# Optimization experiments

Measured on AMD Instinct MI355X. Metric: run time of the kernel, lower is better.

## Reference

```python
import jax, jax.numpy as jnp
import numpy as np

N_EMBED = 288
HEAD_SIZE = 32


def setup_inputs() -> dict:
    key = jax.random.key(0)
    kx, kk, kq, kv = jax.random.split(key, 4)
    B, T, C = 16, 2048, N_EMBED
    scale = 1.0 / np.sqrt(C)
    return {
        "x": jax.random.normal(kx, (B, T, C), dtype=jnp.float32),
        # Linear(n_embed, head_size, bias=False) weights, stored as [C, head_size]
        "Wk": jax.random.normal(kk, (C, HEAD_SIZE), dtype=jnp.float32) * scale,
        "Wq": jax.random.normal(kq, (C, HEAD_SIZE), dtype=jnp.float32) * scale,
        "Wv": jax.random.normal(kv, (C, HEAD_SIZE), dtype=jnp.float32) * scale,
    }


def reference(x, Wk, Wq, Wv):
    # x: [B, T, C]
    k = x @ Wk  # [B, T, hs]
    q = x @ Wq
    v = x @ Wv
    # NOTE: source computes k @ q^T (not q @ k^T) -- reproduce faithfully.
    weights = jnp.einsum("bth,bsh->bts", k, q) * (HEAD_SIZE ** -0.5)  # [B, T, T]
    T = x.shape[1]
    causal = jnp.tril(jnp.ones((T, T), dtype=bool))
    weights = jnp.where(causal, weights, -jnp.inf)
    weights = jax.nn.softmax(weights, axis=-1)
    return weights @ v  # [B, T, hs]
```

## Files before the change

kernel.cpp:

```cpp
#include <hip/hip_runtime.h>

typedef __bf16 bf16;
typedef __attribute__((ext_vector_type(8))) __bf16 bf16x8;
typedef __attribute__((ext_vector_type(4))) float f32x4;

#define BATCH 16
#define SEQ   2048
#define CEMB  288
#define HS    32
#define NROWS (BATCH * SEQ)

#define XSTR 296

__global__ __launch_bounds__(384) void proj_kernel(
    const float* __restrict__ x, const float* __restrict__ Wk,
    const float* __restrict__ Wq, const float* __restrict__ Wv,
    bf16* __restrict__ Kx, bf16* __restrict__ Qm, bf16* __restrict__ VT)
{
    __shared__ __align__(16) bf16 Xl[32 * XSTR];

    const int tid  = threadIdx.x;
    const int wv   = tid >> 6;
    const int lane = tid & 63;
    const int quad = lane >> 4;
    const int ln   = lane & 15;
    const int dsel = wv >> 1;
    const int half = wv & 1;

    const float SCALE = 0.25519486439582695f;

    const float* Wsrc = (dsel == 0) ? Wk : ((dsel == 1) ? Wq : Wv);
    const float mul = (dsel == 0) ? SCALE : 1.0f;
    bf16x8 wfrag[9];
    for (int kc = 0; kc < 9; ++kc) {
        bf16x8 f;
#pragma unroll
        for (int j = 0; j < 8; ++j) {
            float w = Wsrc[(kc * 32 + quad * 8 + j) * HS + half * 16 + ln];
            f[j] = (bf16)(w * mul);
        }
        wfrag[kc] = f;
    }

    const int wgRowBase = blockIdx.x * 128;
    for (int it = 0; it < 4; ++it) {
        __syncthreads();
        const int rb = wgRowBase + it * 32;
#pragma unroll
        for (int i = 0; i < 6; ++i) {
            int f = tid + 384 * i;
            int row = f / 72;
            int c4  = f - row * 72;
            f32x4 v = ((const f32x4*)x)[(rb + row) * 72 + c4];
            bf16* d = &Xl[row * XSTR + c4 * 4];
            d[0] = (bf16)v[0]; d[1] = (bf16)v[1];
            d[2] = (bf16)v[2]; d[3] = (bf16)v[3];
        }
        __syncthreads();

#pragma unroll
        for (int m = 0; m < 2; ++m) {
            f32x4 acc = {0.f, 0.f, 0.f, 0.f};
#pragma unroll
            for (int kc = 0; kc < 9; ++kc) {
                bf16x8 a = *(const bf16x8*)&Xl[(m * 16 + ln) * XSTR + kc * 32 + quad * 8];
                acc = __builtin_amdgcn_mfma_f32_16x16x32_bf16(a, wfrag[kc], acc, 0, 0, 0);
            }
#pragma unroll
            for (int reg = 0; reg < 4; ++reg) {
                int gr = rb + m * 16 + quad * 4 + reg;
                bf16 val = (bf16)acc[reg];
                if (dsel == 0) {
                    Kx[gr * HS + half * 16 + ln] = val;
                } else if (dsel == 1) {
                    Qm[gr * HS + half * 16 + ln] = val;
                } else {
                    VT[(gr >> 11) * (HS * SEQ) + (half * 16 + ln) * SEQ + (gr & 2047)] = val;
                }
            }
        }
    }
}

#define QSTR 40
#define PSTR 56

__constant__ unsigned char MAP_TILE[40] = {
    4,5,6,7, 8,8,9,9, 10,10,11,11, 12,12,12, 13,13,13, 14,14,14, 15,15,15,
    3,7,11,15, 2,6,10,14, 1,5,9,13, 0,4,8,12 };
__constant__ unsigned char MAP_CHUNK[40] = {
    0,0,0,0, 0,1,0,1, 0,1,0,1, 0,1,2, 0,1,2, 0,1,2, 0,1,2,
    0,1,2,3, 0,1,2,3, 0,1,2,3, 0,1,2,3 };

__global__ __launch_bounds__(256) void attn_kernel(
    const bf16* __restrict__ Kx, const bf16* __restrict__ Qm,
    const bf16* __restrict__ VT,
    float* __restrict__ Opart, float* __restrict__ Lpart)
{
    __shared__ __align__(16) bf16 qT[32 * QSTR];
    __shared__ __align__(16) bf16 vT[32 * QSTR];
    __shared__ __align__(16) bf16 Pl[4][2][16 * PSTR];

    const int tid  = threadIdx.x;
    const int w    = tid >> 6;
    const int lane = tid & 63;
    const int quad = lane >> 4;
    const int ln   = lane & 15;

    const int bid   = blockIdx.x;
    const int b     = bid & 15;
    const int u     = bid >> 4;
    const int tile  = MAP_TILE[u];
    const int chunk = MAP_CHUNK[u];
    const int t0    = tile * 128;
    const int cs    = chunk * 512;
    const int ce    = min(cs + 512, t0 + 128);

    const bf16* Kb = Kx + b * SEQ * HS;
    const bf16* Qb = Qm + b * SEQ * HS;
    const bf16* Vb = VT + b * HS * SEQ;

    int tsub[2];
    bf16x8 kfrag[2];
#pragma unroll
    for (int m = 0; m < 2; ++m) {
        tsub[m] = t0 + w * 32 + m * 16;
        kfrag[m] = *(const bf16x8*)&Kb[(tsub[m] + ln) * HS + quad * 8];
    }
    bf16x8 ones;
#pragma unroll
    for (int j = 0; j < 8; ++j) ones[j] = (bf16)1.0f;

    f32x4 Of[2][2] = {};
    f32x4 Lf[2]    = {};

    for (int s0 = cs; s0 < ce; s0 += 32) {
        __syncthreads();
        if (tid < 128) {
            int sr = tid >> 2, h8 = (tid & 3) * 8;
            *(bf16x8*)&qT[sr * QSTR + h8] = *(const bf16x8*)&Qb[(s0 + sr) * HS + h8];
        } else {
            int t2 = tid - 128;
            int hr = t2 >> 2, s8 = (t2 & 3) * 8;
            *(bf16x8*)&vT[hr * QSTR + s8] = *(const bf16x8*)&Vb[hr * SEQ + s0 + s8];
        }
        __syncthreads();

#pragma unroll
        for (int m = 0; m < 2; ++m) {
            if (s0 >= tsub[m] + 16) continue;
            const bool diag = (s0 + 31 > tsub[m]);

            f32x4 S[2];
#pragma unroll
            for (int ss = 0; ss < 2; ++ss) {
                bf16x8 qf = *(const bf16x8*)&qT[(ss * 16 + ln) * QSTR + quad * 8];
                f32x4 z = {0.f, 0.f, 0.f, 0.f};
                S[ss] = __builtin_amdgcn_mfma_f32_16x16x32_bf16(kfrag[m], qf, z, 0, 0, 0);
            }

            bf16* P = &Pl[w][m][0];
#pragma unroll
            for (int ss = 0; ss < 2; ++ss) {
#pragma unroll
                for (int reg = 0; reg < 4; ++reg) {
                    float p = __builtin_amdgcn_exp2f(S[ss][reg]);
                    if (diag) {
                        int s = s0 + ss * 16 + ln;
                        int t = tsub[m] + quad * 4 + reg;
                        p = (s <= t) ? p : 0.0f;
                    }
                    P[(quad * 4 + reg) * PSTR + ss * 16 + ln] = (bf16)p;
                }
            }

            bf16x8 ap = *(const bf16x8*)&P[ln * PSTR + quad * 8];
            bf16x8 v0 = *(const bf16x8*)&vT[ln * QSTR + quad * 8];
            bf16x8 v1 = *(const bf16x8*)&vT[(16 + ln) * QSTR + quad * 8];
            Of[m][0] = __builtin_amdgcn_mfma_f32_16x16x32_bf16(ap, v0, Of[m][0], 0, 0, 0);
            Of[m][1] = __builtin_amdgcn_mfma_f32_16x16x32_bf16(ap, v1, Of[m][1], 0, 0, 0);
            Lf[m]    = __builtin_amdgcn_mfma_f32_16x16x32_bf16(ap, ones, Lf[m], 0, 0, 0);
        }
    }

#pragma unroll
    for (int m = 0; m < 2; ++m) {
        if (cs >= tsub[m] + 16) continue;
#pragma unroll
        for (int reg = 0; reg < 4; ++reg) {
            int gr = b * SEQ + tsub[m] + quad * 4 + reg;
            float* od = Opart + ((size_t)chunk * NROWS + gr) * HS;
            od[ln]      = Of[m][0][reg];
            od[16 + ln] = Of[m][1][reg];
            if (ln == 0) Lpart[chunk * NROWS + gr] = Lf[m][reg];
        }
    }
}

__global__ __launch_bounds__(256) void combine_kernel(
    const float* __restrict__ Opart, const float* __restrict__ Lpart,
    float* __restrict__ out)
{
    int idx = blockIdx.x * 256 + threadIdx.x;
    int gr = idx >> 3, h4 = idx & 7;
    int t  = gr & 2047;
    int nc = (t >> 9) + 1;
    f32x4 acc = {0.f, 0.f, 0.f, 0.f};
    float l = 0.f;
    for (int c = 0; c < nc; ++c) {
        acc += ((const f32x4*)Opart)[((size_t)c * NROWS + gr) * 8 + h4];
        l   += Lpart[c * NROWS + gr];
    }
    f32x4 r = acc / l;
    ((f32x4*)out)[idx] = r;
}

extern "C" void kernel_launch(void* const* d_in, const int* in_sizes, int n_in,
                              void* d_out, int out_size, void* d_ws, size_t ws_size,
                              hipStream_t stream) {
    (void)in_sizes; (void)n_in; (void)out_size; (void)ws_size;
    const float* x  = (const float*)d_in[0];
    const float* Wk = (const float*)d_in[1];
    const float* Wq = (const float*)d_in[2];
    const float* Wv = (const float*)d_in[3];

    char* ws = (char*)d_ws;
    bf16*  Kx    = (bf16*)(ws);
    bf16*  Qm    = (bf16*)(ws + 2097152);
    bf16*  VT    = (bf16*)(ws + 4194304);
    float* Opart = (float*)(ws + 6291456);
    float* Lpart = (float*)(ws + 23068672);
    float* out   = (float*)d_out;

    hipLaunchKernelGGL(proj_kernel, dim3(256), dim3(384), 0, stream,
                       x, Wk, Wq, Wv, Kx, Qm, VT);
    hipLaunchKernelGGL(attn_kernel, dim3(640), dim3(256), 0, stream,
                       Kx, Qm, VT, Opart, Lpart);
    hipLaunchKernelGGL(combine_kernel, dim3(1024), dim3(256), 0, stream,
                       Opart, Lpart, out);
}
```

Measured before the change: 111.8 us.

## Give each wave its own query tile and keep P in registers via 16x16x16 MFMA

The attention kernel now assigns each wave an independent 32-row tile and chunk, so workgroup-wide barriers and shared staging of Q/V are gone. K/Q/V fragments are loaded directly from global memory, with the next block prefetched into registers. When the 16x16x16 bf16 MFMA is available, the exp'd score fragment is fed straight back as the A operand, with no LDS round trip for P. Fully masked sub-blocks are skipped. The projection kernel also launches twice as many workgroups with half the rows each, to spread work more widely. The trade-offs are more global loads per wave (no sharing through LDS) and more register use.

After: 119.5 us. 1.07x slower.

```diff
diff --git a/kernel.cpp b/kernel.cpp
--- a/kernel.cpp
+++ b/kernel.cpp
@@ -2,6 +2,8 @@
 
 typedef __bf16 bf16;
 typedef __attribute__((ext_vector_type(8))) __bf16 bf16x8;
+typedef __attribute__((ext_vector_type(4))) __bf16 bf16x4;
+typedef __attribute__((ext_vector_type(4))) short s16x4;
 typedef __attribute__((ext_vector_type(4))) float f32x4;
 
 #define BATCH 16
@@ -9,6 +11,13 @@
 #define CEMB  288
 #define HS    32
 #define NROWS (BATCH * SEQ)
+
+#if __has_builtin(__builtin_amdgcn_mfma_f32_16x16x16bf16_1k)
+#define HAVE_MFMA16 1
+#define MFMA16(a, b, c) __builtin_amdgcn_mfma_f32_16x16x16bf16_1k((a), (b), (c), 0, 0, 0)
+#else
+#define HAVE_MFMA16 0
+#endif
 
 #define XSTR 296
 
@@ -42,8 +51,8 @@
         wfrag[kc] = f;
     }
 
-    const int wgRowBase = blockIdx.x * 128;
-    for (int it = 0; it < 4; ++it) {
+    const int wgRowBase = blockIdx.x * 64;
+    for (int it = 0; it < 2; ++it) {
         __syncthreads();
         const int rb = wgRowBase + it * 32;
 #pragma unroll
@@ -82,24 +91,16 @@
     }
 }
 
-#define QSTR 40
-#define PSTR 56
-
-__constant__ unsigned char MAP_TILE[40] = {
-    4,5,6,7, 8,8,9,9, 10,10,11,11, 12,12,12, 13,13,13, 14,14,14, 15,15,15,
-    3,7,11,15, 2,6,10,14, 1,5,9,13, 0,4,8,12 };
-__constant__ unsigned char MAP_CHUNK[40] = {
-    0,0,0,0, 0,1,0,1, 0,1,0,1, 0,1,2, 0,1,2, 0,1,2, 0,1,2,
-    0,1,2,3, 0,1,2,3, 0,1,2,3, 0,1,2,3 };
+#define PSTR 40
 
 __global__ __launch_bounds__(256) void attn_kernel(
     const bf16* __restrict__ Kx, const bf16* __restrict__ Qm,
     const bf16* __restrict__ VT,
     float* __restrict__ Opart, float* __restrict__ Lpart)
 {
-    __shared__ __align__(16) bf16 qT[32 * QSTR];
-    __shared__ __align__(16) bf16 vT[32 * QSTR];
-    __shared__ __align__(16) bf16 Pl[4][2][16 * PSTR];
+#if !HAVE_MFMA16
+    __shared__ __align__(16) bf16 Pl[4][16 * PSTR];
+#endif
 
     const int tid  = threadIdx.x;
     const int w    = tid >> 6;
@@ -107,92 +108,150 @@
     const int quad = lane >> 4;
     const int ln   = lane & 15;
 
-    const int bid   = blockIdx.x;
-    const int b     = bid & 15;
-    const int u     = bid >> 4;
-    const int tile  = MAP_TILE[u];
-    const int chunk = MAP_CHUNK[u];
-    const int t0    = tile * 128;
-    const int cs    = chunk * 512;
-    const int ce    = min(cs + 512, t0 + 128);
+    const int b = blockIdx.x & 15;
+    const int j = (blockIdx.x >> 4) * 4 + w;
+    int c, tt;
+    if (j < 64)       { c = 0; tt = 63 - j; }
+    else if (j < 112) { c = 1; tt = 63 - (j - 64); }
+    else if (j < 144) { c = 2; tt = 63 - (j - 112); }
+    else              { c = 3; tt = 63 - (j - 144); }
+
+    const int tlo = tt * 32;
+    const int cs  = c * 512;
+    const int ce  = (cs + 512 < tlo + 32) ? (cs + 512) : (tlo + 32);
 
     const bf16* Kb = Kx + b * SEQ * HS;
     const bf16* Qb = Qm + b * SEQ * HS;
     const bf16* Vb = VT + b * HS * SEQ;
 
-    int tsub[2];
-    bf16x8 kfrag[2];
-#pragma unroll
-    for (int m = 0; m < 2; ++m) {
-        tsub[m] = t0 + w * 32 + m * 16;
-        kfrag[m] = *(const bf16x8*)&Kb[(tsub[m] + ln) * HS + quad * 8];
-    }
-    bf16x8 ones;
-#pragma unroll
-    for (int j = 0; j < 8; ++j) ones[j] = (bf16)1.0f;
+    bf16x8 kfragB[2];
+#pragma unroll
+    for (int th = 0; th < 2; ++th)
+        kfragB[th] = *(const bf16x8*)&Kb[(tlo + th * 16 + ln) * HS + quad * 8];
 
     f32x4 Of[2][2] = {};
     f32x4 Lf[2]    = {};
 
+#if HAVE_MFMA16
+    s16x4 ones4;
+#pragma unroll
+    for (int i = 0; i < 4; ++i) ones4[i] = (short)0x3F80;
+
+    bf16x8 qf[2];
+    s16x4  vb[2][2];
+    qf[0] = *(const bf16x8*)&Qb[(cs + ln) * HS + quad * 8];
+    qf[1] = *(const bf16x8*)&Qb[(cs + 16 + ln) * HS + quad * 8];
+#pragma unroll
+    for (int sh = 0; sh < 2; ++sh)
+#pragma unroll
+        for (int hh = 0; hh < 2; ++hh)
+            vb[sh][hh] = *(const s16x4*)&Vb[(hh * 16 + ln) * SEQ + cs + sh * 16 + quad * 4];
+
     for (int s0 = cs; s0 < ce; s0 += 32) {
-        __syncthreads();
-        if (tid < 128) {
-            int sr = tid >> 2, h8 = (tid & 3) * 8;
-            *(bf16x8*)&qT[sr * QSTR + h8] = *(const bf16x8*)&Qb[(s0 + sr) * HS + h8];
-        } else {
-            int t2 = tid - 128;
-            int hr = t2 >> 2, s8 = (t2 & 3) * 8;
-            *(bf16x8*)&vT[hr * QSTR + s8] = *(const bf16x8*)&Vb[hr * SEQ + s0 + s8];
-        }
-        __syncthreads();
-
-#pragma unroll
-        for (int m = 0; m < 2; ++m) {
-            if (s0 >= tsub[m] + 16) continue;
-            const bool diag = (s0 + 31 > tsub[m]);
-
-            f32x4 S[2];
-#pragma unroll
-            for (int ss = 0; ss < 2; ++ss) {
-                bf16x8 qf = *(const bf16x8*)&qT[(ss * 16 + ln) * QSTR + quad * 8];
+        const int sn = (s0 + 32 < ce) ? (s0 + 32) : s0;
+        bf16x8 qn0 = *(const bf16x8*)&Qb[(sn + ln) * HS + quad * 8];
+        bf16x8 qn1 = *(const bf16x8*)&Qb[(sn + 16 + ln) * HS + quad * 8];
+        s16x4  vn[2][2];
+#pragma unroll
+        for (int sh = 0; sh < 2; ++sh)
+#pragma unroll
+            for (int hh = 0; hh < 2; ++hh)
+                vn[sh][hh] = *(const s16x4*)&Vb[(hh * 16 + ln) * SEQ + sn + sh * 16 + quad * 4];
+
+#pragma unroll
+        for (int th = 0; th < 2; ++th) {
+            const int tbase = tlo + th * 16;
+            if (s0 >= tbase + 16) continue;
+            const int tcol = tbase + ln;
+#pragma unroll
+            for (int sh = 0; sh < 2; ++sh) {
+                const int sb = s0 + sh * 16;
+                if (sb >= tbase + 16) continue;
+                const bool dmask = (sb == tbase);
                 f32x4 z = {0.f, 0.f, 0.f, 0.f};
-                S[ss] = __builtin_amdgcn_mfma_f32_16x16x32_bf16(kfrag[m], qf, z, 0, 0, 0);
+                f32x4 S = __builtin_amdgcn_mfma_f32_16x16x32_bf16(
+                              qf[sh], kfragB[th], z, 0, 0, 0);
+                const int sbase = sb + quad * 4;
+                bf16x4 pk;
+#pragma unroll
+                for (int r = 0; r < 4; ++r) {
+                    float p = __builtin_amdgcn_exp2f(S[r]);
+                    if (dmask) p = (sbase + r <= tcol) ? p : 0.0f;
+                    pk[r] = (bf16)p;
+                }
+                s16x4 ap = __builtin_bit_cast(s16x4, pk);
+                Of[th][0] = MFMA16(ap, vb[sh][0], Of[th][0]);
+                Of[th][1] = MFMA16(ap, vb[sh][1], Of[th][1]);
+                Lf[th]    = MFMA16(ap, ones4,     Lf[th]);
             }
-
-            bf16* P = &Pl[w][m][0];
-#pragma unroll
-            for (int ss = 0; ss < 2; ++ss) {
-#pragma unroll
-                for (int reg = 0; reg < 4; ++reg) {
-                    float p = __builtin_amdgcn_exp2f(S[ss][reg]);
-                    if (diag) {
-                        int s = s0 + ss * 16 + ln;
-                        int t = tsub[m] + quad * 4 + reg;
-                        p = (s <= t) ? p : 0.0f;
-                    }
-                    P[(quad * 4 + reg) * PSTR + ss * 16 + ln] = (bf16)p;
+        }
+        qf[0] = qn0; qf[1] = qn1;
+#pragma unroll
+        for (int sh = 0; sh < 2; ++sh)
+#pragma unroll
+            for (int hh = 0; hh < 2; ++hh)
+                vb[sh][hh] = vn[sh][hh];
+    }
+#else
+    bf16x8 ones;
+#pragma unroll
+    for (int i = 0; i < 8; ++i) ones[i] = (bf16)1.0f;
+    bf16* P = &Pl[w][0];
+
+    bf16x8 qf[2], vf[2];
+    qf[0] = *(const bf16x8*)&Qb[(cs + ln) * HS + quad * 8];
+    qf[1] = *(const bf16x8*)&Qb[(cs + 16 + ln) * HS + quad * 8];
+    vf[0] = *(const bf16x8*)&Vb[ln * SEQ + cs + quad * 8];
+    vf[1] = *(const bf16x8*)&Vb[(16 + ln) * SEQ + cs + quad * 8];
+
+    for (int s0 = cs; s0 < ce; s0 += 32) {
+        const int sn = (s0 + 32 < ce) ? (s0 + 32) : s0;
+        bf16x8 qn0 = *(const bf16x8*)&Qb[(sn + ln) * HS + quad * 8];
+        bf16x8 qn1 = *(const bf16x8*)&Qb[(sn + 16 + ln) * HS + quad * 8];
+        bf16x8 vn0 = *(const bf16x8*)&Vb[ln * SEQ + sn + quad * 8];
+        bf16x8 vn1 = *(const bf16x8*)&Vb[(16 + ln) * SEQ + sn + quad * 8];
+
+#pragma unroll
+        for (int th = 0; th < 2; ++th) {
+            const int tbase = tlo + th * 16;
+            if (s0 >= tbase + 16) continue;
+            const bool diag = (s0 + 31 >= tbase);
+            const int tcol = tbase + ln;
+#pragma unroll
+            for (int sh = 0; sh < 2; ++sh) {
+                f32x4 z = {0.f, 0.f, 0.f, 0.f};
+                f32x4 S = __builtin_amdgcn_mfma_f32_16x16x32_bf16(
+                              qf[sh], kfragB[th], z, 0, 0, 0);
+                const int sbase = s0 + sh * 16 + quad * 4;
+                bf16x4 pk;
+#pragma unroll
+                for (int r = 0; r < 4; ++r) {
+                    float p = __builtin_amdgcn_exp2f(S[r]);
+                    if (diag) p = (sbase + r <= tcol) ? p : 0.0f;
+                    pk[r] = (bf16)p;
                 }
+                *(bf16x4*)&P[ln * PSTR + sh * 16 + quad * 4] = pk;
             }
-
+            asm volatile("" ::: "memory");
             bf16x8 ap = *(const bf16x8*)&P[ln * PSTR + quad * 8];
-            bf16x8 v0 = *(const bf16x8*)&vT[ln * QSTR + quad * 8];
-            bf16x8 v1 = *(const bf16x8*)&vT[(16 + ln) * QSTR + quad * 8];
-            Of[m][0] = __builtin_amdgcn_mfma_f32_16x16x32_bf16(ap, v0, Of[m][0], 0, 0, 0);
-            Of[m][1] = __builtin_amdgcn_mfma_f32_16x16x32_bf16(ap, v1, Of[m][1], 0, 0, 0);
-            Lf[m]    = __builtin_amdgcn_mfma_f32_16x16x32_bf16(ap, ones, Lf[m], 0, 0, 0);
-        }
-    }
-
-#pragma unroll
-    for (int m = 0; m < 2; ++m) {
-        if (cs >= tsub[m] + 16) continue;
+            asm volatile("" ::: "memory");
+            Of[th][0] = __builtin_amdgcn_mfma_f32_16x16x32_bf16(ap, vf[0], Of[th][0], 0, 0, 0);
+            Of[th][1] = __builtin_amdgcn_mfma_f32_16x16x32_bf16(ap, vf[1], Of[th][1], 0, 0, 0);
+            Lf[th]    = __builtin_amdgcn_mfma_f32_16x16x32_bf16(ap, ones,  Lf[th],    0, 0, 0);
+        }
+        qf[0] = qn0; qf[1] = qn1; vf[0] = vn0; vf[1] = vn1;
+    }
+#endif
+
+#pragma unroll
+    for (int th = 0; th < 2; ++th) {
 #pragma unroll
         for (int reg = 0; reg < 4; ++reg) {
-            int gr = b * SEQ + tsub[m] + quad * 4 + reg;
-            float* od = Opart + ((size_t)chunk * NROWS + gr) * HS;
-            od[ln]      = Of[m][0][reg];
-            od[16 + ln] = Of[m][1][reg];
-            if (ln == 0) Lpart[chunk * NROWS + gr] = Lf[m][reg];
+            int gr = b * SEQ + tlo + th * 16 + quad * 4 + reg;
+            float* od = Opart + ((size_t)c * NROWS + gr) * HS;
+            od[ln]      = Of[th][0][reg];
+            od[16 + ln] = Of[th][1][reg];
+            if (ln == 0) Lpart[c * NROWS + gr] = Lf[th][reg];
         }
     }
 }
@@ -232,7 +291,7 @@
     float* Lpart = (float*)(ws + 23068672);
     float* out   = (float*)d_out;
 
-    hipLaunchKernelGGL(proj_kernel, dim3(256), dim3(384), 0, stream,
+    hipLaunchKernelGGL(proj_kernel, dim3(512), dim3(384), 0, stream,
                        x, Wk, Wq, Wv, Kx, Qm, VT);
     hipLaunchKernelGGL(attn_kernel, dim3(640), dim3(256), 0, stream,
                        Kx, Qm, VT, Opart, Lpart);
```
